# Performance work log

Measured on AMD Instinct MI355X. Metric: run time of the kernel, lower is better.

Reference implementation:

```python
import jax, jax.numpy as jnp
import numpy as np

N_NODES = 100000
N_EDGES = 1600000
D_IN = 64
D_OUT = 64
N_AGGR = 2   # mean, std
N_SCAL = 3   # identity, amplification, attenuation
EPS = 1e-7


def setup_inputs() -> dict:
    key = jax.random.key(0)
    ks = jax.random.split(key, 6)
    x = jax.random.normal(ks[0], (N_NODES, D_IN), dtype=jnp.float32)
    edge_row = jax.random.randint(ks[1], (N_EDGES,), 0, N_NODES)  # dst nodes
    edge_col = jax.random.randint(ks[2], (N_EDGES,), 0, N_NODES)  # src nodes
    # glorot init for linear weights, stored as [out, in] like torch.nn.Linear
    g = np.sqrt(6.0 / (D_IN + D_OUT))
    pre_w = jax.random.uniform(ks[3], (N_AGGR, N_SCAL, D_OUT, D_IN),
                               minval=-g, maxval=g, dtype=jnp.float32)
    lin_w = jax.random.uniform(ks[4], (D_OUT, D_IN), minval=-g, maxval=g,
                               dtype=jnp.float32)
    bias = jnp.zeros((D_OUT,), dtype=jnp.float32)
    # avg_deg['log'] = mean over nodes of log(deg+1); use expected value ~log(17)
    avg_deg_log = jnp.asarray(np.log(17.0), dtype=jnp.float32)
    return {"x": x, "edge_row": edge_row, "edge_col": edge_col,
            "pre_w": pre_w, "lin_w": lin_w, "bias": bias,
            "avg_deg_log": avg_deg_log}


def reference(x, edge_row, edge_col, pre_w, lin_w, bias, avg_deg_log):
    n = x.shape[0]
    # deg = adj_t.storage.rowcount(): number of edges per destination node
    deg = jax.ops.segment_sum(jnp.ones_like(edge_row, dtype=x.dtype),
                              edge_row, num_segments=n)[:, None]  # [N,1]
    # Two SpMM passes: adj_t @ x and adj_t @ x**2 (sum over source neighbors)
    xj = x[edge_col]                                             # [E,D]
    s1 = jax.ops.segment_sum(xj, edge_row, num_segments=n)       # [N,D]
    s2 = jax.ops.segment_sum(xj * xj, edge_row, num_segments=n)  # [N,D]
    mean = s1
    std = jnp.sqrt(jax.nn.relu(s2 - s1 * s1) + EPS)
    agg = jnp.stack([mean, std])                                 # [2,N,D]
    # 6 per-head projections: heads ordered as product(aggregators, scalers)
    proj = jnp.einsum('and,asod->asno', agg, pre_w)              # [2,3,N,O]
    logd = jnp.log(deg + 1.0)                                    # [N,1]
    factors = jnp.stack([
        jnp.ones_like(logd),            # identity
        logd / avg_deg_log,             # amplification
        avg_deg_log / (logd + EPS),     # attenuation
    ])                                                           # [3,N,1]
    out = (proj * factors[None]).sum(axis=(0, 1))                # sum over heads
    out = out + x @ lin_w.T + bias
    return out
```

## Files before the change

### kernel.cpp

```cpp
#include <hip/hip_runtime.h>
#include <cmath>

constexpr int D = 64;
constexpr int KTOT = 448;
constexpr int KSTEPS = 14;
constexpr int ZROW = 456;
constexpr int NBMAX = 256;

typedef __attribute__((ext_vector_type(8))) short bf16x8;
typedef __attribute__((ext_vector_type(4))) float f32x4;

static __device__ inline ushort bfq(float f) {
  unsigned u = __builtin_bit_cast(unsigned, f);
  return (ushort)((u + 0x7FFFu + ((u >> 16) & 1u)) >> 16);
}
static __device__ inline float b2f(ushort h) {
  return __builtin_bit_cast(float, (unsigned)h << 16);
}

__global__ void __launch_bounds__(256)
kA_prep(const float* __restrict__ x, const int* __restrict__ erow,
        int* __restrict__ bucket_cnt, ushort* __restrict__ xh,
        const float* __restrict__ pre_w, const float* __restrict__ lin_w,
        float* __restrict__ Wt, ushort* __restrict__ Bfrag,
        int ne, int total) {
  __shared__ int h[NBMAX];
  int t = threadIdx.x;
  h[t] = 0;
  __syncthreads();

  int base = blockIdx.x * 2048 + t * 8;
  if (base + 7 < total) {
    const float4* xp = (const float4*)(x + base);
    float4 v0 = xp[0], v1 = xp[1];
    uint4 o;
    o.x = (unsigned)bfq(v0.x) | ((unsigned)bfq(v0.y) << 16);
    o.y = (unsigned)bfq(v0.z) | ((unsigned)bfq(v0.w) << 16);
    o.z = (unsigned)bfq(v1.x) | ((unsigned)bfq(v1.y) << 16);
    o.w = (unsigned)bfq(v1.z) | ((unsigned)bfq(v1.w) << 16);
    *(uint4*)(xh + base) = o;
  } else {
    for (int u = 0; u < 8 && base + u < total; ++u) xh[base + u] = bfq(x[base + u]);
  }

  int idx = blockIdx.x * 256 + t;
  if (idx < KTOT * 64) {
    int k = idx >> 6, o = idx & 63;
    int slot = k >> 6, d = k & 63;
    Wt[idx] = (slot < 6) ? pre_w[slot * 4096 + o * 64 + d] : lin_w[o * 64 + d];
    int j = idx & 7, lane = (idx >> 3) & 63, ot = (idx >> 9) & 3, ks = idx >> 11;
    int kk = ks * 32 + (lane >> 4) * 8 + j;
    int oo = ot * 16 + (lane & 15);
    int s2 = kk >> 6, d2 = kk & 63;
    float v = (s2 < 6) ? pre_w[s2 * 4096 + oo * 64 + d2] : lin_w[oo * 64 + d2];
    Bfrag[idx] = bfq(v);
  }

  int ebase = blockIdx.x * 2048;
  if (ebase < ne) {
    int elim = ne - ebase; if (elim > 2048) elim = 2048;
    for (int u = t * 8; u < t * 8 + 8; ++u)
      if (u < elim) atomicAdd(&h[erow[ebase + u] >> 9], 1);
    __syncthreads();
    if (h[t] > 0) atomicAdd(&bucket_cnt[t], h[t]);
  }
}

__global__ void kC_scan(const int* __restrict__ bucket_cnt, int* __restrict__ bbase,
                        int* __restrict__ bcur, int nbk) {
  __shared__ int ts[NBMAX];
  int t = threadIdx.x;
  int v = (t < nbk) ? bucket_cnt[t] : 0;
  ts[t] = v;
  __syncthreads();
  for (int off = 1; off < NBMAX; off <<= 1) {
    int u = (t >= off) ? ts[t - off] : 0;
    __syncthreads();
    ts[t] += u;
    __syncthreads();
  }
  if (t < nbk) {
    bbase[t + 1] = ts[t];
    bcur[t] = ts[t] - v;
    if (t == 0) bbase[0] = 0;
  }
}

#define BTILE 8192
__global__ void __launch_bounds__(256)
kD_binpass(const int* __restrict__ erow, const int* __restrict__ ecol,
           int* __restrict__ bcur, unsigned* __restrict__ pairs, int ne) {
  __shared__ int h[NBMAX], gb[NBMAX], h2[NBMAX];
  int t = threadIdx.x;
  h[t] = 0; h2[t] = 0;
  __syncthreads();
  int base = blockIdx.x * BTILE;
  int lim = ne - base; if (lim > BTILE) lim = BTILE;
  for (int k = t; k < lim; k += 256)
    atomicAdd(&h[erow[base + k] >> 9], 1);
  __syncthreads();
  if (h[t] > 0) gb[t] = atomicAdd(&bcur[t], h[t]);
  __syncthreads();
  for (int k = t; k < lim; k += 256) {
    int dst = erow[base + k];
    int src = ecol[base + k];
    int b = dst >> 9;
    int r = atomicAdd(&h2[b], 1);
    pairs[gb[b] + r] = ((unsigned)(dst & 511) << 17) | (unsigned)src;
  }
}

__global__ void __launch_bounds__(512)
kE_within(const unsigned* __restrict__ pairs, const int* __restrict__ bbase,
          int* __restrict__ rowptr, int* __restrict__ esrc, int nn) {
  __shared__ int lcnt[512], ts[512];
  int b = blockIdx.x;
  int t = threadIdx.x;
  int nstart = b << 9;
  int s = bbase[b], e = bbase[b + 1];
  int m = e - s;
  lcnt[t] = 0;
  __syncthreads();
  for (int i = t; i < m; i += 512)
    atomicAdd(&lcnt[pairs[s + i] >> 17], 1);
  __syncthreads();
  int v = lcnt[t];
  ts[t] = v;
  __syncthreads();
  for (int off = 1; off < 512; off <<= 1) {
    int u = (t >= off) ? ts[t - off] : 0;
    __syncthreads();
    ts[t] += u;
    __syncthreads();
  }
  int incl = ts[t];
  int n = nstart + t;
  if (n < nn) rowptr[n + 1] = s + incl;
  if (b == 0 && t == 0) rowptr[0] = 0;
  lcnt[t] = s + incl - v;
  __syncthreads();
  for (int i = t; i < m; i += 512) {
    unsigned w = pairs[s + i];
    int p = atomicAdd(&lcnt[w >> 17], 1);
    esrc[p] = (int)(w & 0x1FFFFu);
  }
}

static __device__ inline void chunk_acc(const ushort* __restrict__ xh, int sv,
                                        int cnt, int lane, float& a1, float& a2) {
  int k = 0;
  for (; k + 15 < cnt; k += 16) {
    float v[16];
#pragma unroll
    for (int u = 0; u < 16; ++u)
      v[u] = b2f(xh[__shfl(sv, k + u) * 64 + lane]);
#pragma unroll
    for (int u = 0; u < 16; ++u) { a1 += v[u]; a2 = fmaf(v[u], v[u], a2); }
  }
  for (; k + 3 < cnt; k += 4) {
    float v[4];
#pragma unroll
    for (int u = 0; u < 4; ++u)
      v[u] = b2f(xh[__shfl(sv, k + u) * 64 + lane]);
#pragma unroll
    for (int u = 0; u < 4; ++u) { a1 += v[u]; a2 = fmaf(v[u], v[u], a2); }
  }
  for (; k < cnt; ++k) {
    float v = b2f(xh[__shfl(sv, k) * 64 + lane]);
    a1 += v; a2 = fmaf(v, v, a2);
  }
}

__global__ void __launch_bounds__(256, 6)
k_agg_dense(const ushort* __restrict__ xh,
            const float* __restrict__ x,
            const int* __restrict__ rowptr,
            const int* __restrict__ esrc,
            const ushort* __restrict__ Bfrag,
            const float* __restrict__ bias,
            const float* __restrict__ avgp,
            float* __restrict__ out, int nn) {
  __shared__ __align__(16) ushort zs[16 * ZROW];
  const float avg = avgp[0];
  const int wave = threadIdx.x >> 6, lane = threadIdx.x & 63;
  const int n0 = blockIdx.x * 16;
  const int nw = n0 + wave * 4;

  int rpv = (lane < 5) ? rowptr[nw + lane] : 0;
  int e0 = __shfl(rpv, 0), e1 = __shfl(rpv, 1), e2 = __shfl(rpv, 2),
      e3 = __shfl(rpv, 3), e4 = __shfl(rpv, 4);
  int sv0 = (e0 + lane < e1) ? esrc[e0 + lane] : 0;
  int sv1 = (e1 + lane < e2) ? esrc[e1 + lane] : 0;
  int sv2 = (e2 + lane < e3) ? esrc[e2 + lane] : 0;
  int sv3 = (e3 + lane < e4) ? esrc[e3 + lane] : 0;

#define DO_NODE(J, SJ, EJ, SVJ)                                           \
  {                                                                       \
    int n = nw + J;                                                       \
    float a1 = 0.f, a2 = 0.f;                                             \
    int nb = EJ - SJ; if (nb > 64) nb = 64;                               \
    chunk_acc(xh, SVJ, nb, lane, a1, a2);                                 \
    for (int base = SJ + 64; base < EJ; base += 64) {                     \
      int c = EJ - base; if (c > 64) c = 64;                              \
      int sv = (base + lane < EJ) ? esrc[base + lane] : 0;                \
      chunk_acc(xh, sv, c, lane, a1, a2);                                 \
    }                                                                     \
    float m = a1;                                                         \
    float sd = sqrtf(fmaxf(a2 - m * m, 0.f) + 1e-7f);                     \
    float degf = (float)(EJ - SJ);                                        \
    float logd = logf(degf + 1.f);                                        \
    float f2 = logd / avg;                                                \
    float f3 = avg / (logd + 1e-7f);                                      \
    float xv = (n < nn) ? x[n * 64 + lane] : 0.f;                         \
    if (n >= nn) { m = 0.f; sd = 0.f; f2 = 0.f; f3 = 0.f; }               \
    ushort* zr = zs + (wave * 4 + J) * ZROW;                              \
    zr[lane]       = bfq(m);                                              \
    zr[64 + lane]  = bfq(m * f2);                                         \
    zr[128 + lane] = bfq(m * f3);                                         \
    zr[192 + lane] = bfq(sd);                                             \
    zr[256 + lane] = bfq(sd * f2);                                        \
    zr[320 + lane] = bfq(sd * f3);                                        \
    zr[384 + lane] = bfq(xv);                                             \
  }
  DO_NODE(0, e0, e1, sv0)
  DO_NODE(1, e1, e2, sv1)
  DO_NODE(2, e2, e3, sv2)
  DO_NODE(3, e3, e4, sv3)
#undef DO_NODE

  __syncthreads();

  const int r = lane & 15, kg = lane >> 4;
  const ushort* za = zs + r * ZROW + kg * 8;
  const ushort* bp = Bfrag + (wave * 64 + lane) * 8;
  f32x4 acc = {0.f, 0.f, 0.f, 0.f};
#pragma unroll
  for (int ks = 0; ks < KSTEPS; ++ks) {
    bf16x8 a = *(const bf16x8*)(za + ks * 32);
    bf16x8 b = *(const bf16x8*)(bp + ks * 2048);
    acc = __builtin_amdgcn_mfma_f32_16x16x32_bf16(a, b, acc, 0, 0, 0);
  }
  float bc = bias[wave * 16 + r];
#pragma unroll
  for (int i = 0; i < 4; ++i) {
    int n = n0 + kg * 4 + i;
    if (n < nn) out[n * 64 + wave * 16 + r] = acc[i] + bc;
  }
}

__global__ void k_fixup(const int* __restrict__ rowptr, const float* __restrict__ x,
                        const float* __restrict__ Wt, const float* __restrict__ bias,
                        const float* __restrict__ avgp, float* __restrict__ out, int nn) {
  int n = blockIdx.x * 256 + threadIdx.x;
  if (n >= nn) return;
  if (rowptr[n + 1] != rowptr[n]) return;
  float avg = avgp[0];
  float sd = sqrtf(1e-7f);
  float f3 = avg / 1e-7f;
  for (int o = 0; o < 64; ++o) {
    float acc = bias[o];
    for (int d = 0; d < 64; ++d) {
      acc += sd * Wt[(192 + d) * 64 + o];
      acc += sd * f3 * Wt[(320 + d) * 64 + o];
      acc += x[n * 64 + d] * Wt[(384 + d) * 64 + o];
    }
    out[n * 64 + o] = acc;
  }
}

extern "C" void kernel_launch(void* const* d_in, const int* in_sizes, int n_in,
                              void* d_out, int out_size, void* d_ws, size_t ws_size,
                              hipStream_t stream) {
  const float* x     = (const float*)d_in[0];
  const int*   erow  = (const int*)d_in[1];
  const int*   ecol  = (const int*)d_in[2];
  const float* pre_w = (const float*)d_in[3];
  const float* lin_w = (const float*)d_in[4];
  const float* bias  = (const float*)d_in[5];
  const float* avgp  = (const float*)d_in[6];
  float* out = (float*)d_out;

  int nn = in_sizes[0] / 64;
  int ne = in_sizes[1];
  int total = nn * 64;
  int nbk = (nn + 511) / 512;

  char* w = (char*)d_ws;
  auto align = [](size_t v) { return (v + 255) & ~(size_t)255; };
  size_t off = 0;
  ushort* xh     = (ushort*)(w + off); off = align(off + (size_t)total * 2);
  int* esrc      = (int*)(w + off); off = align(off + (size_t)ne * 4);
  unsigned* prs  = (unsigned*)(w + off); off = align(off + (size_t)ne * 4);
  int* rowptr    = (int*)(w + off); off = align(off + (size_t)(nn + 1) * 4);
  int* bucket_cnt= (int*)(w + off); size_t bc_off = off; off = align(off + NBMAX * 4);
  int* bbase     = (int*)(w + off); off = align(off + (NBMAX + 1) * 4);
  int* bcur      = (int*)(w + off); off = align(off + NBMAX * 4);
  float* Wt      = (float*)(w + off); off = align(off + (size_t)KTOT * 64 * 4);
  ushort* Bfr    = (ushort*)(w + off); off = align(off + (size_t)KSTEPS * 4 * 64 * 8 * 2);
  (void)ws_size;

  hipMemsetAsync(w + bc_off, 0, NBMAX * 4, stream);

  int gA = (total + 2047) / 2048;
  kA_prep<<<gA, 256, 0, stream>>>(x, erow, bucket_cnt, xh, pre_w, lin_w, Wt, Bfr,
                                  ne, total);
  kC_scan<<<1, NBMAX, 0, stream>>>(bucket_cnt, bbase, bcur, nbk);
  kD_binpass<<<(ne + BTILE - 1) / BTILE, 256, 0, stream>>>(erow, ecol, bcur, prs, ne);
  kE_within<<<nbk, 512, 0, stream>>>(prs, bbase, rowptr, esrc, nn);
  k_agg_dense<<<(nn + 15) / 16, 256, 0, stream>>>(xh, x, rowptr, esrc, Bfr, bias,
                                                  avgp, out, nn);
  k_fixup<<<(nn + 255) / 256, 256, 0, stream>>>(rowptr, x, Wt, bias, avgp, out, nn);
}
```

Measured before the change: 204.9 us.

## Gather packed bf16 pairs per lane, fold fixup into aggregation, drop global atomics

Measured after the change: 310.9 us. 51.7% more time.

```diff
diff --git a/kernel.cpp b/kernel.cpp
--- a/kernel.cpp
+++ b/kernel.cpp
@@ -1,7 +1,6 @@
 #include <hip/hip_runtime.h>
 #include <cmath>
 
-constexpr int D = 64;
 constexpr int KTOT = 448;
 constexpr int KSTEPS = 14;
 constexpr int ZROW = 456;
@@ -17,10 +16,13 @@
 static __device__ inline float b2f(ushort h) {
   return __builtin_bit_cast(float, (unsigned)h << 16);
 }
+static __device__ inline unsigned pk2(float a, float b) {
+  return (unsigned)bfq(a) | ((unsigned)bfq(b) << 16);
+}
 
 __global__ void __launch_bounds__(256)
 kA_prep(const float* __restrict__ x, const int* __restrict__ erow,
-        int* __restrict__ bucket_cnt, ushort* __restrict__ xh,
+        int* __restrict__ cmat, ushort* __restrict__ xh,
         const float* __restrict__ pre_w, const float* __restrict__ lin_w,
         float* __restrict__ Wt, ushort* __restrict__ Bfrag,
         int ne, int total) {
@@ -34,13 +36,11 @@
     const float4* xp = (const float4*)(x + base);
     float4 v0 = xp[0], v1 = xp[1];
     uint4 o;
-    o.x = (unsigned)bfq(v0.x) | ((unsigned)bfq(v0.y) << 16);
-    o.y = (unsigned)bfq(v0.z) | ((unsigned)bfq(v0.w) << 16);
-    o.z = (unsigned)bfq(v1.x) | ((unsigned)bfq(v1.y) << 16);
-    o.w = (unsigned)bfq(v1.z) | ((unsigned)bfq(v1.w) << 16);
+    o.x = pk2(v0.x, v0.y);
+    o.y = pk2(v0.z, v0.w);
+    o.z = pk2(v1.x, v1.y);
+    o.w = pk2(v1.z, v1.w);
     *(uint4*)(xh + base) = o;
-  } else {
-    for (int u = 0; u < 8 && base + u < total; ++u) xh[base + u] = bfq(x[base + u]);
   }
 
   int idx = blockIdx.x * 256 + t;
@@ -59,20 +59,23 @@
   int ebase = blockIdx.x * 2048;
   if (ebase < ne) {
     int elim = ne - ebase; if (elim > 2048) elim = 2048;
-    for (int u = t * 8; u < t * 8 + 8; ++u)
-      if (u < elim) atomicAdd(&h[erow[ebase + u] >> 9], 1);
-    __syncthreads();
-    if (h[t] > 0) atomicAdd(&bucket_cnt[t], h[t]);
-  }
-}
-
-__global__ void kC_scan(const int* __restrict__ bucket_cnt, int* __restrict__ bbase,
-                        int* __restrict__ bcur, int nbk) {
+    for (int u = t; u < elim; u += 256)
+      atomicAdd(&h[erow[ebase + u] >> 9], 1);
+    __syncthreads();
+    cmat[blockIdx.x * NBMAX + t] = h[t];
+  }
+}
+
+__global__ void __launch_bounds__(NBMAX)
+kC_scan(const int* __restrict__ cmat, int ntiles,
+        int* __restrict__ bbase, int* __restrict__ bcur, int nbk) {
   __shared__ int ts[NBMAX];
   int t = threadIdx.x;
-  int v = (t < nbk) ? bucket_cnt[t] : 0;
-  ts[t] = v;
-  __syncthreads();
+  int s = 0;
+  for (int i = 0; i < ntiles; ++i) s += cmat[i * NBMAX + t];
+  ts[t] = s;
+  __syncthreads();
+  int v = s;
   for (int off = 1; off < NBMAX; off <<= 1) {
     int u = (t >= off) ? ts[t - off] : 0;
     __syncthreads();
@@ -146,45 +149,63 @@
   }
 }
 
-static __device__ inline void chunk_acc(const ushort* __restrict__ xh, int sv,
-                                        int cnt, int lane, float& a1, float& a2) {
+static __device__ inline void chunk_pair(const unsigned* __restrict__ xh32, int sv,
+                                         int cnt, int m, int half,
+                                         float& alo, float& ahi,
+                                         float& blo, float& bhi) {
   int k = 0;
   for (; k + 15 < cnt; k += 16) {
-    float v[16];
-#pragma unroll
-    for (int u = 0; u < 16; ++u)
-      v[u] = b2f(xh[__shfl(sv, k + u) * 64 + lane]);
-#pragma unroll
-    for (int u = 0; u < 16; ++u) { a1 += v[u]; a2 = fmaf(v[u], v[u], a2); }
-  }
-  for (; k + 3 < cnt; k += 4) {
-    float v[4];
-#pragma unroll
-    for (int u = 0; u < 4; ++u)
-      v[u] = b2f(xh[__shfl(sv, k + u) * 64 + lane]);
-#pragma unroll
-    for (int u = 0; u < 4; ++u) { a1 += v[u]; a2 = fmaf(v[u], v[u], a2); }
-  }
-  for (; k < cnt; ++k) {
-    float v = b2f(xh[__shfl(sv, k) * 64 + lane]);
-    a1 += v; a2 = fmaf(v, v, a2);
+    unsigned u[8];
+#pragma unroll
+    for (int p = 0; p < 8; ++p) {
+      int i0 = __shfl(sv, k + 2 * p);
+      int i1 = __shfl(sv, k + 2 * p + 1);
+      int row = half ? i1 : i0;
+      u[p] = xh32[row * 32 + m];
+    }
+#pragma unroll
+    for (int p = 0; p < 8; ++p) {
+      float flo = __builtin_bit_cast(float, u[p] << 16);
+      float fhi = __builtin_bit_cast(float, u[p] & 0xFFFF0000u);
+      alo += flo; blo = fmaf(flo, flo, blo);
+      ahi += fhi; bhi = fmaf(fhi, fhi, bhi);
+    }
+  }
+  for (; k + 1 < cnt; k += 2) {
+    int i0 = __shfl(sv, k), i1 = __shfl(sv, k + 1);
+    int row = half ? i1 : i0;
+    unsigned u = xh32[row * 32 + m];
+    float flo = __builtin_bit_cast(float, u << 16);
+    float fhi = __builtin_bit_cast(float, u & 0xFFFF0000u);
+    alo += flo; blo = fmaf(flo, flo, blo);
+    ahi += fhi; bhi = fmaf(fhi, fhi, bhi);
+  }
+  if (k < cnt) {
+    int i0 = __shfl(sv, k);
+    unsigned u = half ? 0u : xh32[i0 * 32 + m];
+    float flo = __builtin_bit_cast(float, u << 16);
+    float fhi = __builtin_bit_cast(float, u & 0xFFFF0000u);
+    alo += flo; blo = fmaf(flo, flo, blo);
+    ahi += fhi; bhi = fmaf(fhi, fhi, bhi);
   }
 }
 
 __global__ void __launch_bounds__(256, 6)
 k_agg_dense(const ushort* __restrict__ xh,
-            const float* __restrict__ x,
             const int* __restrict__ rowptr,
             const int* __restrict__ esrc,
             const ushort* __restrict__ Bfrag,
+            const float* __restrict__ Wt,
             const float* __restrict__ bias,
             const float* __restrict__ avgp,
             float* __restrict__ out, int nn) {
   __shared__ __align__(16) ushort zs[16 * ZROW];
   const float avg = avgp[0];
   const int wave = threadIdx.x >> 6, lane = threadIdx.x & 63;
+  const int m = lane & 31, half = lane >> 5;
   const int n0 = blockIdx.x * 16;
   const int nw = n0 + wave * 4;
+  const unsigned* xh32 = (const unsigned*)xh;
 
   int rpv = (lane < 5) ? rowptr[nw + lane] : 0;
   int e0 = __shfl(rpv, 0), e1 = __shfl(rpv, 1), e2 = __shfl(rpv, 2),
@@ -194,33 +215,39 @@
   int sv2 = (e2 + lane < e3) ? esrc[e2 + lane] : 0;
   int sv3 = (e3 + lane < e4) ? esrc[e3 + lane] : 0;
 
-#define DO_NODE(J, SJ, EJ, SVJ)                                           \
-  {                                                                       \
-    int n = nw + J;                                                       \
-    float a1 = 0.f, a2 = 0.f;                                             \
-    int nb = EJ - SJ; if (nb > 64) nb = 64;                               \
-    chunk_acc(xh, SVJ, nb, lane, a1, a2);                                 \
-    for (int base = SJ + 64; base < EJ; base += 64) {                     \
-      int c = EJ - base; if (c > 64) c = 64;                              \
-      int sv = (base + lane < EJ) ? esrc[base + lane] : 0;                \
-      chunk_acc(xh, sv, c, lane, a1, a2);                                 \
-    }                                                                     \
-    float m = a1;                                                         \
-    float sd = sqrtf(fmaxf(a2 - m * m, 0.f) + 1e-7f);                     \
-    float degf = (float)(EJ - SJ);                                        \
-    float logd = logf(degf + 1.f);                                        \
-    float f2 = logd / avg;                                                \
-    float f3 = avg / (logd + 1e-7f);                                      \
-    float xv = (n < nn) ? x[n * 64 + lane] : 0.f;                         \
-    if (n >= nn) { m = 0.f; sd = 0.f; f2 = 0.f; f3 = 0.f; }               \
-    ushort* zr = zs + (wave * 4 + J) * ZROW;                              \
-    zr[lane]       = bfq(m);                                              \
-    zr[64 + lane]  = bfq(m * f2);                                         \
-    zr[128 + lane] = bfq(m * f3);                                         \
-    zr[192 + lane] = bfq(sd);                                             \
-    zr[256 + lane] = bfq(sd * f2);                                        \
-    zr[320 + lane] = bfq(sd * f3);                                        \
-    zr[384 + lane] = bfq(xv);                                             \
+  int zmask = 0;
+
+#define DO_NODE(J, SJ, EJ, SVJ)                                              \
+  {                                                                          \
+    int n = nw + J;                                                          \
+    float alo = 0.f, ahi = 0.f, blo = 0.f, bhi = 0.f;                        \
+    int nb = EJ - SJ; if (nb > 64) nb = 64;                                  \
+    chunk_pair(xh32, SVJ, nb, m, half, alo, ahi, blo, bhi);                  \
+    for (int base = SJ + 64; base < EJ; base += 64) {                        \
+      int c = EJ - base; if (c > 64) c = 64;                                 \
+      int sv = (base + lane < EJ) ? esrc[base + lane] : 0;                   \
+      chunk_pair(xh32, sv, c, m, half, alo, ahi, blo, bhi);                  \
+    }                                                                        \
+    alo += __shfl_xor(alo, 32); ahi += __shfl_xor(ahi, 32);                  \
+    blo += __shfl_xor(blo, 32); bhi += __shfl_xor(bhi, 32);                  \
+    float sdlo = sqrtf(fmaxf(blo - alo * alo, 0.f) + 1e-7f);                 \
+    float sdhi = sqrtf(fmaxf(bhi - ahi * ahi, 0.f) + 1e-7f);                 \
+    int deg = EJ - SJ;                                                       \
+    if (deg == 0) zmask |= (1 << J);                                         \
+    float logd = logf((float)deg + 1.f);                                     \
+    float f2 = logd / avg;                                                   \
+    float f3 = avg / (logd + 1e-7f);                                         \
+    unsigned xu = xh32[n * 32 + m];                                          \
+    if (half == 0) {                                                         \
+      unsigned* zr = (unsigned*)(zs + (wave * 4 + J) * ZROW);                \
+      zr[m]        = pk2(alo, ahi);                                          \
+      zr[32 + m]   = pk2(alo * f2, ahi * f2);                                \
+      zr[64 + m]   = pk2(alo * f3, ahi * f3);                                \
+      zr[96 + m]   = pk2(sdlo, sdhi);                                        \
+      zr[128 + m]  = pk2(sdlo * f2, sdhi * f2);                              \
+      zr[160 + m]  = pk2(sdlo * f3, sdhi * f3);                              \
+      zr[192 + m]  = xu;                                                     \
+    }                                                                        \
   }
   DO_NODE(0, e0, e1, sv0)
   DO_NODE(1, e1, e2, sv1)
@@ -246,25 +273,26 @@
     int n = n0 + kg * 4 + i;
     if (n < nn) out[n * 64 + wave * 16 + r] = acc[i] + bc;
   }
-}
-
-__global__ void k_fixup(const int* __restrict__ rowptr, const float* __restrict__ x,
-                        const float* __restrict__ Wt, const float* __restrict__ bias,
-                        const float* __restrict__ avgp, float* __restrict__ out, int nn) {
-  int n = blockIdx.x * 256 + threadIdx.x;
-  if (n >= nn) return;
-  if (rowptr[n + 1] != rowptr[n]) return;
-  float avg = avgp[0];
-  float sd = sqrtf(1e-7f);
-  float f3 = avg / 1e-7f;
-  for (int o = 0; o < 64; ++o) {
-    float acc = bias[o];
-    for (int d = 0; d < 64; ++d) {
-      acc += sd * Wt[(192 + d) * 64 + o];
-      acc += sd * f3 * Wt[(320 + d) * 64 + o];
-      acc += x[n * 64 + d] * Wt[(384 + d) * 64 + o];
+
+  if (__syncthreads_or(zmask)) {
+    int eo[5] = {e0, e1, e2, e3, e4};
+#pragma unroll
+    for (int J = 0; J < 4; ++J) {
+      int n = nw + J;
+      if ((zmask >> J) & 1 && n < nn) {
+        float sd0 = sqrtf(1e-7f);
+        float f3z = avg / 1e-7f;
+        float accx = bias[lane];
+        for (int d = 0; d < 64; ++d) {
+          float xd = b2f(xh[n * 64 + d]);
+          accx += sd0 * Wt[(192 + d) * 64 + lane]
+                + sd0 * f3z * Wt[(320 + d) * 64 + lane]
+                + xd * Wt[(384 + d) * 64 + lane];
+        }
+        out[n * 64 + lane] = accx;
+      }
+      (void)eo[J];
     }
-    out[n * 64 + o] = acc;
   }
 }
 
@@ -284,6 +312,7 @@
   int ne = in_sizes[1];
   int total = nn * 64;
   int nbk = (nn + 511) / 512;
+  int ntiles = (ne + 2047) / 2048;
 
   char* w = (char*)d_ws;
   auto align = [](size_t v) { return (v + 255) & ~(size_t)255; };
@@ -292,22 +321,19 @@
   int* esrc      = (int*)(w + off); off = align(off + (size_t)ne * 4);
   unsigned* prs  = (unsigned*)(w + off); off = align(off + (size_t)ne * 4);
   int* rowptr    = (int*)(w + off); off = align(off + (size_t)(nn + 1) * 4);
-  int* bucket_cnt= (int*)(w + off); size_t bc_off = off; off = align(off + NBMAX * 4);
+  int* cmat      = (int*)(w + off); off = align(off + (size_t)ntiles * NBMAX * 4);
   int* bbase     = (int*)(w + off); off = align(off + (NBMAX + 1) * 4);
   int* bcur      = (int*)(w + off); off = align(off + NBMAX * 4);
   float* Wt      = (float*)(w + off); off = align(off + (size_t)KTOT * 64 * 4);
   ushort* Bfr    = (ushort*)(w + off); off = align(off + (size_t)KSTEPS * 4 * 64 * 8 * 2);
   (void)ws_size;
 
-  hipMemsetAsync(w + bc_off, 0, NBMAX * 4, stream);
-
   int gA = (total + 2047) / 2048;
-  kA_prep<<<gA, 256, 0, stream>>>(x, erow, bucket_cnt, xh, pre_w, lin_w, Wt, Bfr,
+  kA_prep<<<gA, 256, 0, stream>>>(x, erow, cmat, xh, pre_w, lin_w, Wt, Bfr,
                                   ne, total);
-  kC_scan<<<1, NBMAX, 0, stream>>>(bucket_cnt, bbase, bcur, nbk);
+  kC_scan<<<1, NBMAX, 0, stream>>>(cmat, ntiles, bbase, bcur, nbk);
   kD_binpass<<<(ne + BTILE - 1) / BTILE, 256, 0, stream>>>(erow, ecol, bcur, prs, ne);
   kE_within<<<nbk, 512, 0, stream>>>(prs, bbase, rowptr, esrc, nn);
-  k_agg_dense<<<(nn + 15) / 16, 256, 0, stream>>>(xh, x, rowptr, esrc, Bfr, bias,
+  k_agg_dense<<<(nn + 15) / 16, 256, 0, stream>>>(xh, rowptr, esrc, Bfr, Wt, bias,
                                                   avgp, out, nn);
-  k_fixup<<<(nn + 255) / 256, 256, 0, stream>>>(rowptr, x, Wt, bias, avgp, out, nn);
-}
+}
```
